# Kernel optimization log

Measured on AMD Instinct MI355X. Metric: run time of the kernel, lower is better.

The kernel has to match this reference:

```python
import jax, jax.numpy as jnp
import numpy as np

D_CUT = 5.0   # cosine-cutoff distance
SIZE = 128    # rbf size == hidden_channels (nn_dist size = in_channels)
L = 2         # num_layers
EPS = 0.0     # GIN eps (non-trainable, initial 0)


def _rbf(d):
    # d: (E,) distances -> (E, SIZE) expnorm RBF with cosine cutoff
    d = d[:, None]
    start = float(np.exp(-D_CUT))
    means = jnp.linspace(start, 1.0, SIZE)
    beta = (2.0 / SIZE * (1.0 - start)) ** (-2)
    dc = jnp.minimum(d, D_CUT)
    cutoff = 0.5 * (jnp.cos(dc * jnp.pi / D_CUT) + 1.0)
    return cutoff * jnp.exp(-beta * (jnp.exp(-d) - means) ** 2)


def setup_inputs() -> dict:
    key = jax.random.key(0)
    ks = jax.random.split(key, 40)
    it = iter(range(40))
    def k():
        return ks[next(it)]
    N, H, ED, AS = 100000, 128, 4, 4
    def w(shape, s):
        return jax.random.normal(k(), shape, jnp.float32) * s
    inp = {}
    inp['x_lig'] = jax.random.normal(k(), (N, H), jnp.float32)
    inp['x_pock'] = jax.random.normal(k(), (N, H), jnp.float32)
    for name, E in (('bond', 200000), ('lp', 400000), ('pl', 400000)):
        inp['ei_' + name] = jax.random.randint(k(), (2, E), 0, N, jnp.int32)
        inp['ew_' + name] = jax.random.uniform(k(), (E,), jnp.float32) * D_CUT
        inp['ea_' + name] = jax.random.normal(k(), (E, AS), jnp.float32)
    inp['W0'] = w((3, AS, ED), 0.5)                 # initial per-edge-type lins (no bias)
    inp['Wd'] = w((L, 3, H, 2 * H), H ** -0.5)      # RBFDistanceScaleShift lin
    inp['bd'] = jnp.zeros((L, 3, 2 * H), jnp.float32)
    inp['We'] = w((L, 3, ED, H), 0.5)               # EGINConv.lin (edge_dim -> hidden)
    inp['be'] = jnp.zeros((L, 3, H), jnp.float32)
    inp['W1'] = w((L, 3, H, H), H ** -0.5)          # nn_node MLP layer 1
    inp['b1'] = jnp.zeros((L, 3, H), jnp.float32)
    inp['W2'] = w((L, 3, H, H), H ** -0.5)          # nn_node MLP layer 2
    inp['b2'] = jnp.zeros((L, 3, H), jnp.float32)
    return inp


def reference(x_lig, x_pock, ei_bond, ew_bond, ea_bond, ei_lp, ew_lp, ea_lp,
              ei_pl, ew_pl, ea_pl, W0, Wd, bd, We, be, W1, b1, W2, b2):
    # HeteroEGIN.forward: initial per-edge-type linear on raw edge attrs (bias-free)
    ea0 = ea_bond @ W0[0]
    ea1 = ea_lp @ W0[1]
    ea2 = ea_pl @ W0[2]

    def conv(x_src, x_dst, ei, ew, ea, t, l):
        # EGINConv per edge type t, layer l
        ss = _rbf(ew) @ Wd[l, t] + bd[l, t]            # (E, 2H) scale/shift from distance
        scale, shift = jnp.split(ss, 2, axis=1)
        xj = x_src[ei[0]] + (ea @ We[l, t] + be[l, t])  # gather + edge-attr lin
        msg = jax.nn.relu(xj * scale + shift)           # gated message
        agg = jax.ops.segment_sum(msg, ei[1], num_segments=x_dst.shape[0])
        o = agg + (1.0 + EPS) * x_dst
        return jax.nn.relu(o @ W1[l, t] + b1[l, t]) @ W2[l, t] + b2[l, t]

    for l in range(L):
        # to_hetero: sum conv outputs across edge types per destination node type
        new_lig = (conv(x_lig, x_lig, ei_bond, ew_bond, ea0, 0, l)
                   + conv(x_pock, x_lig, ei_pl, ew_pl, ea2, 2, l))
        new_pock = conv(x_lig, x_pock, ei_lp, ew_lp, ea1, 1, l)
        if l < L - 1:  # BasicGNN: act between layers, none after last (jk=None)
            new_lig = jax.nn.relu(new_lig)
            new_pock = jax.nn.relu(new_pock)
        x_lig, x_pock = new_lig, new_pock
    return jnp.concatenate([x_lig, x_pock], axis=0)
```

## Files before the change

### kernel.cpp

```cpp
#include <hip/hip_runtime.h>
#include <hip/hip_bf16.h>
#include <hip/hip_fp16.h>
#include <cmath>

typedef __attribute__((ext_vector_type(8))) short short8_t;
typedef __attribute__((ext_vector_type(4))) float f32x4;

static __device__ __forceinline__ short f2bs(float f) {
    union { __hip_bfloat16 h; short s; } u;
    u.h = __float2bfloat16(f);
    return u.s;
}
static __device__ __forceinline__ float bs2f(unsigned int us) {
    union { float f; unsigned int i; } u;
    u.i = us << 16;
    return u.f;
}
static __device__ __forceinline__ unsigned int pack2bf(float a, float b) {
    return (unsigned int)(unsigned short)f2bs(a) |
           ((unsigned int)(unsigned short)f2bs(b) << 16);
}
static __device__ __forceinline__ void lds_barrier() {
    asm volatile("s_waitcnt lgkmcnt(0)\n\ts_barrier" ::: "memory");
}

__global__ void pack_kernel(const float* __restrict__ Wd,
                            const float* __restrict__ W1,
                            const float* __restrict__ W2,
                            const float* __restrict__ W0,
                            const float* __restrict__ We,
                            short* __restrict__ pWd,
                            short* __restrict__ pW1,
                            short* __restrict__ pW2,
                            float* __restrict__ Mb)
{
    const int tid = blockIdx.x * blockDim.x + threadIdx.x;
    const int stride = gridDim.x * blockDim.x;
    for (int i = tid; i < 6 * 32768; i += stride) {
        int c = i >> 15, rem = i & 32767;
        int f = rem >> 9, l = (rem >> 3) & 63, j = rem & 7;
        int kk = f >> 4, nt = f & 15;
        int k = kk * 32 + (l >> 4) * 8 + j;
        int n = nt * 16 + (l & 15);
        pWd[i] = f2bs(Wd[(size_t)c * 32768 + k * 256 + n]);
    }
    for (int i = tid; i < 6 * 16384; i += stride) {
        int c = i >> 14, rem = i & 16383;
        int f = rem >> 9, l = (rem >> 3) & 63, j = rem & 7;
        int kk = f >> 3, nt = f & 7;
        int k = kk * 32 + (l >> 4) * 8 + j;
        int n = nt * 16 + (l & 15);
        pW1[i] = f2bs(W1[(size_t)c * 16384 + k * 128 + n]);
        pW2[i] = f2bs(W2[(size_t)c * 16384 + k * 128 + n]);
    }
    for (int i = tid; i < 6 * 512; i += stride) {
        int c = i >> 9, rem = i & 511;
        int a = rem >> 7, h = rem & 127;
        int t = c % 3;
        float m = 0.f;
        #pragma unroll
        for (int j = 0; j < 4; ++j)
            m = fmaf(W0[t * 16 + a * 4 + j], We[(size_t)c * 512 + j * 128 + h], m);
        Mb[i] = m;
    }
}

__global__ void tobf16_kernel(const float* __restrict__ a, const float* __restrict__ b,
                              unsigned short* __restrict__ oa, unsigned short* __restrict__ ob,
                              int n4)
{
    int i = blockIdx.x * blockDim.x + threadIdx.x;
    const int stride = gridDim.x * blockDim.x;
    for (; i < n4; i += stride) {
        float4 va = ((const float4*)a)[i];
        uint2 pa; pa.x = pack2bf(va.x, va.y); pa.y = pack2bf(va.z, va.w);
        ((uint2*)oa)[i] = pa;
        float4 vb = ((const float4*)b)[i];
        uint2 pb; pb.x = pack2bf(vb.x, vb.y); pb.y = pack2bf(vb.z, vb.w);
        ((uint2*)ob)[i] = pb;
    }
}

__global__ __launch_bounds__(512, 2)
void edge_mfma_kernel(
    const unsigned short* __restrict__ xsb,
    const int* __restrict__ ei,
    const float* __restrict__ ew, const float* __restrict__ ea,
    const short* __restrict__ pWd, const float* __restrict__ bd,
    const float* __restrict__ Mb, const float* __restrict__ be,
    __half2* __restrict__ agg, int E, int ntiles,
    float rs, float rstep, float rbeta)
{
    __shared__ short sRbf[64 * 128];
    __shared__ __half sSS[64 * 256];

    const int t = threadIdx.x;
    const int lane = t & 63;
    const int w = t >> 6;
    const int l15 = lane & 15;
    const int l4 = lane >> 4;

    short8_t bfrag[4][2];
    #pragma unroll
    for (int kk = 0; kk < 4; ++kk)
        #pragma unroll
        for (int i = 0; i < 2; ++i)
            bfrag[kk][i] = *(const short8_t*)&pWd[((kk * 16 + 2 * w + i) * 64 + lane) * 8];
    float bdv[2];
    #pragma unroll
    for (int i = 0; i < 2; ++i) bdv[i] = bd[(2 * w + i) * 16 + l15];
    const float be0 = be[2 * lane], be1 = be[2 * lane + 1];
    float ma0[4], ma1[4];
    #pragma unroll
    for (int a = 0; a < 4; ++a) {
        ma0[a] = Mb[a * 128 + 2 * lane];
        ma1[a] = Mb[a * 128 + 2 * lane + 1];
    }

    const int stride = gridDim.x;
    int tile = blockIdx.x;
    if (tile >= ntiles) return;

    float dd_c; int dst_c; float4 ea_c;
    unsigned int gx[8];
    {
        const int e0 = tile << 6;
        int eL = e0 + lane;
        int eLc = eL < E ? eL : E - 1;
        dd_c = ew[eLc];
        int es = e0 + w * 8 + (lane & 7);
        int esv = es < E ? es : E - 1;
        dst_c = (es < E) ? ei[E + esv] : -1;
        int src_c = ei[esv];
        ea_c = *(const float4*)&ea[(size_t)esv * 4];
        #pragma unroll
        for (int r = 0; r < 8; ++r) {
            int srn = __shfl(src_c, r);
            gx[r] = *(const unsigned int*)&xsb[(size_t)srn * 128 + lane * 2];
        }
    }

    for (; tile < ntiles; tile += stride) {
        const float edv = __expf(-dd_c);
        const float dcc = fminf(dd_c, 5.0f);
        const float cutv = 0.5f * (__cosf(dcc * 0.62831853071795864769f) + 1.0f);
        {
            char* base = (char*)sRbf + lane * 256;
            #pragma unroll
            for (int c = 0; c < 2; ++c) {
                short8_t v;
                #pragma unroll
                for (int j = 0; j < 8; ++j) {
                    float mean = rs + (float)(w * 16 + c * 8 + j) * rstep;
                    float diff = edv - mean;
                    v[j] = f2bs(cutv * __expf(-rbeta * diff * diff));
                }
                *(short8_t*)(base + ((w * 32 + c * 16) ^ ((lane & 7) << 4))) = v;
            }
        }
        unsigned int xjr[8];
        #pragma unroll
        for (int r = 0; r < 8; ++r) {
            float ea0 = __shfl(ea_c.x, r), ea1 = __shfl(ea_c.y, r);
            float ea2 = __shfl(ea_c.z, r), ea3 = __shfl(ea_c.w, r);
            unsigned int g = gx[r];
            float x0 = bs2f(g & 0xffffu), x1 = bs2f(g >> 16);
            float o0 = x0 + be0 + ea0 * ma0[0] + ea1 * ma0[1] + ea2 * ma0[2] + ea3 * ma0[3];
            float o1 = x1 + be1 + ea0 * ma1[0] + ea1 * ma1[1] + ea2 * ma1[2] + ea3 * ma1[3];
            xjr[r] = pack2bf(o0, o1);
        }

        lds_barrier();

        const int ntile = tile + stride;
        const bool has_next = ntile < ntiles;
        float dd_n = 0.f; int dst_n = -1; int src_n = 0;
        float4 ea_n = {0.f, 0.f, 0.f, 0.f};
        if (has_next) {
            const int e0n = ntile << 6;
            int eL = e0n + lane;
            int eLc = eL < E ? eL : E - 1;
            dd_n = ew[eLc];
            int es = e0n + w * 8 + (lane & 7);
            int esv = es < E ? es : E - 1;
            dst_n = (es < E) ? ei[E + esv] : -1;
            src_n = ei[esv];
            ea_n = *(const float4*)&ea[(size_t)esv * 4];
        }
        __builtin_amdgcn_sched_barrier(0);

        f32x4 acc[4][2];
        #pragma unroll
        for (int m = 0; m < 4; ++m) {
            acc[m][0] = (f32x4){0.f, 0.f, 0.f, 0.f};
            acc[m][1] = (f32x4){0.f, 0.f, 0.f, 0.f};
        }
        #pragma unroll
        for (int kk = 0; kk < 4; ++kk) {
            short8_t af[4];
            #pragma unroll
            for (int m = 0; m < 4; ++m) {
                int row = m * 16 + l15;
                int byte = row * 256 + ((kk * 64 + l4 * 16) ^ ((row & 7) << 4));
                af[m] = *(const short8_t*)((const char*)sRbf + byte);
            }
            #pragma unroll
            for (int m = 0; m < 4; ++m)
                #pragma unroll
                for (int i = 0; i < 2; ++i)
                    acc[m][i] = __builtin_amdgcn_mfma_f32_16x16x32_bf16(
                        af[m], bfrag[kk][i], acc[m][i], 0, 0, 0);
        }

        #pragma unroll
        for (int m = 0; m < 4; ++m)
            #pragma unroll
            for (int i = 0; i < 2; ++i) {
                int col = (2 * w + i) * 16 + l15;
                #pragma unroll
                for (int r = 0; r < 4; ++r) {
                    int row = m * 16 + l4 * 4 + r;
                    int byte = row * 512 + ((col * 2) ^ ((row & 7) << 4));
                    *(__half*)((char*)sSS + byte) = __float2half(acc[m][i][r] + bdv[i]);
                }
            }

        if (has_next) {
            #pragma unroll
            for (int r = 0; r < 8; ++r) {
                int srn = __shfl(src_n, r);
                gx[r] = *(const unsigned int*)&xsb[(size_t)srn * 128 + lane * 2];
            }
        }
        const int dst_f = dst_c;
        dd_c = dd_n; dst_c = dst_n; ea_c = ea_n;

        lds_barrier();

        #pragma unroll
        for (int r = 0; r < 8; ++r) {
            int e = 8 * w + r;
            int dst = __shfl(dst_f, r);
            unsigned int sc = *(const unsigned int*)
                ((const char*)sSS + e * 512 + ((lane * 4) ^ ((e & 7) << 4)));
            unsigned int sh = *(const unsigned int*)
                ((const char*)sSS + e * 512 + ((256 + lane * 4) ^ ((e & 7) << 4)));
            float2 scf = __half22float2(*(const __half2*)&sc);
            float2 shf = __half22float2(*(const __half2*)&sh);
            unsigned int g = xjr[r];
            float x0 = bs2f(g & 0xffffu), x1 = bs2f(g >> 16);
            float m0 = fmaxf(fmaf(x0, scf.x, shf.x), 0.0f);
            float m1 = fmaxf(fmaf(x1, scf.y, shf.y), 0.0f);
            __half2 hv = __floats2half2_rn(m0, m1);
            unsigned int hbits = *(unsigned int*)&hv;
            if (dst >= 0 && hbits != 0u)
                unsafeAtomicAdd(agg + (size_t)dst * 64 + lane, hv);
        }
    }
}

__global__ __launch_bounds__(256)
void node_mfma_kernel(
    const __half2* __restrict__ agg,
    const float* __restrict__ xdf, const unsigned short* __restrict__ xdb,
    const short* __restrict__ pW1, const float* __restrict__ b1,
    const short* __restrict__ pW2, const float* __restrict__ b2,
    float* __restrict__ outf, unsigned short* __restrict__ outb,
    int N, int ntiles, int accumulate, int relu_out)
{
    __shared__ short sA[64 * 128];
    __shared__ short sH[64 * 128];

    const int t = threadIdx.x;
    const int lane = t & 63;
    const int w = t >> 6;
    const int l15 = lane & 15;
    const int l4 = lane >> 4;

    short8_t w1f[4][2], w2f[4][2];
    #pragma unroll
    for (int kk = 0; kk < 4; ++kk)
        #pragma unroll
        for (int p = 0; p < 2; ++p) {
            int nt = 2 * w + p;
            w1f[kk][p] = *(const short8_t*)&pW1[((kk * 8 + nt) * 64 + lane) * 8];
            w2f[kk][p] = *(const short8_t*)&pW2[((kk * 8 + nt) * 64 + lane) * 8];
        }
    float b1v[2], b2v[2];
    #pragma unroll
    for (int p = 0; p < 2; ++p) {
        int col = (2 * w + p) * 16 + l15;
        b1v[p] = b1[col];
        b2v[p] = b2[col];
    }

    for (int tile = blockIdx.x; tile < ntiles; tile += gridDim.x) {
        const int n0 = tile << 6;
        #pragma unroll
        for (int i = 0; i < 4; ++i) {
            int idx = i * 256 + t;
            int row = idx >> 4, c8 = idx & 15;
            int gr = n0 + row; if (gr >= N) gr = N - 1;
            union { float4 f; __half2 h[4]; } ar;
            ar.f = ((const float4*)agg)[(size_t)gr * 16 + c8];
            float xv[8];
            if (xdf) {
                float4 x0 = ((const float4*)xdf)[(size_t)gr * 32 + c8 * 2];
                float4 x1 = ((const float4*)xdf)[(size_t)gr * 32 + c8 * 2 + 1];
                xv[0] = x0.x; xv[1] = x0.y; xv[2] = x0.z; xv[3] = x0.w;
                xv[4] = x1.x; xv[5] = x1.y; xv[6] = x1.z; xv[7] = x1.w;
            } else {
                uint4 xr = ((const uint4*)xdb)[(size_t)gr * 16 + c8];
                xv[0] = bs2f(xr.x & 0xffffu); xv[1] = bs2f(xr.x >> 16);
                xv[2] = bs2f(xr.y & 0xffffu); xv[3] = bs2f(xr.y >> 16);
                xv[4] = bs2f(xr.z & 0xffffu); xv[5] = bs2f(xr.z >> 16);
                xv[6] = bs2f(xr.w & 0xffffu); xv[7] = bs2f(xr.w >> 16);
            }
            short8_t v;
            #pragma unroll
            for (int j = 0; j < 4; ++j) {
                float2 a2 = __half22float2(ar.h[j]);
                v[2 * j]     = f2bs(a2.x + xv[2 * j]);
                v[2 * j + 1] = f2bs(a2.y + xv[2 * j + 1]);
            }
            int byte = row * 256 + ((c8 * 16) ^ ((row & 7) << 4));
            *(short8_t*)((char*)sA + byte) = v;
        }
        lds_barrier();

        f32x4 acc[4][2];
        #pragma unroll
        for (int m = 0; m < 4; ++m) {
            acc[m][0] = (f32x4){0.f, 0.f, 0.f, 0.f};
            acc[m][1] = (f32x4){0.f, 0.f, 0.f, 0.f};
        }
        #pragma unroll
        for (int kk = 0; kk < 4; ++kk) {
            short8_t af[4];
            #pragma unroll
            for (int m = 0; m < 4; ++m) {
                int row = m * 16 + l15;
                int byte = row * 256 + ((kk * 64 + l4 * 16) ^ ((row & 7) << 4));
                af[m] = *(const short8_t*)((const char*)sA + byte);
            }
            #pragma unroll
            for (int m = 0; m < 4; ++m)
                #pragma unroll
                for (int p = 0; p < 2; ++p)
                    acc[m][p] = __builtin_amdgcn_mfma_f32_16x16x32_bf16(
                        af[m], w1f[kk][p], acc[m][p], 0, 0, 0);
        }
        #pragma unroll
        for (int m = 0; m < 4; ++m)
            #pragma unroll
            for (int p = 0; p < 2; ++p) {
                int col = (2 * w + p) * 16 + l15;
                #pragma unroll
                for (int r = 0; r < 4; ++r) {
                    int row = m * 16 + l4 * 4 + r;
                    short hs = f2bs(fmaxf(acc[m][p][r] + b1v[p], 0.f));
                    int byte = row * 256 + ((col * 2) ^ ((row & 7) << 4));
                    *(short*)((char*)sH + byte) = hs;
                }
            }
        lds_barrier();

        f32x4 acc2[4][2];
        #pragma unroll
        for (int m = 0; m < 4; ++m) {
            acc2[m][0] = (f32x4){0.f, 0.f, 0.f, 0.f};
            acc2[m][1] = (f32x4){0.f, 0.f, 0.f, 0.f};
        }
        #pragma unroll
        for (int kk = 0; kk < 4; ++kk) {
            short8_t af[4];
            #pragma unroll
            for (int m = 0; m < 4; ++m) {
                int row = m * 16 + l15;
                int byte = row * 256 + ((kk * 64 + l4 * 16) ^ ((row & 7) << 4));
                af[m] = *(const short8_t*)((const char*)sH + byte);
            }
            #pragma unroll
            for (int m = 0; m < 4; ++m)
                #pragma unroll
                for (int p = 0; p < 2; ++p)
                    acc2[m][p] = __builtin_amdgcn_mfma_f32_16x16x32_bf16(
                        af[m], w2f[kk][p], acc2[m][p], 0, 0, 0);
        }
        #pragma unroll
        for (int m = 0; m < 4; ++m)
            #pragma unroll
            for (int p = 0; p < 2; ++p) {
                int col = (2 * w + p) * 16 + l15;
                #pragma unroll
                for (int r = 0; r < 4; ++r) {
                    int row = n0 + m * 16 + l4 * 4 + r;
                    if (row < N) {
                        float v = acc2[m][p][r] + b2v[p];
                        if (outf) {
                            float* op = &outf[(size_t)row * 128 + col];
                            if (accumulate) v += *op;
                            if (relu_out) v = fmaxf(v, 0.f);
                            *op = v;
                        } else {
                            unsigned short* op = &outb[(size_t)row * 128 + col];
                            if (accumulate) v += bs2f((unsigned int)*op);
                            if (relu_out) v = fmaxf(v, 0.f);
                            *op = (unsigned short)f2bs(v);
                        }
                    }
                }
            }
    }
}

extern "C" void kernel_launch(void* const* d_in, const int* in_sizes, int n_in,
                              void* d_out, int out_size, void* d_ws, size_t ws_size,
                              hipStream_t stream)
{
    const float* x_lig   = (const float*)d_in[0];
    const float* x_pock  = (const float*)d_in[1];
    const int*   ei_bond = (const int*)d_in[2];
    const float* ew_bond = (const float*)d_in[3];
    const float* ea_bond = (const float*)d_in[4];
    const int*   ei_lp   = (const int*)d_in[5];
    const float* ew_lp   = (const float*)d_in[6];
    const float* ea_lp   = (const float*)d_in[7];
    const int*   ei_pl   = (const int*)d_in[8];
    const float* ew_pl   = (const float*)d_in[9];
    const float* ea_pl   = (const float*)d_in[10];
    const float* W0 = (const float*)d_in[11];
    const float* Wd = (const float*)d_in[12];
    const float* bd = (const float*)d_in[13];
    const float* We = (const float*)d_in[14];
    const float* be = (const float*)d_in[15];
    const float* W1 = (const float*)d_in[16];
    const float* b1 = (const float*)d_in[17];
    const float* W2 = (const float*)d_in[18];
    const float* b2 = (const float*)d_in[19];

    const int H = 128;
    const int N = in_sizes[0] / H;
    const int E_bond = in_sizes[3];
    const int E_lp   = in_sizes[6];
    const int E_pl   = in_sizes[9];

    unsigned short* A  = (unsigned short*)d_ws;
    unsigned short* Bb = A  + (size_t)N * H;
    unsigned short* C  = Bb + (size_t)N * H;
    __half* agg = (__half*)(C + (size_t)N * H);
    short* pWd  = (short*)(agg + (size_t)N * H);
    short* pW1s = pWd + 6 * 32768;
    short* pW2s = pW1s + 6 * 16384;
    float* Mb   = (float*)(pW2s + 6 * 16384);

    float* outL = (float*)d_out;
    float* outP = outL + (size_t)N * H;

    const int capE = 2 * 256;
    const int capN = 4 * 256;

    tobf16_kernel<<<512, 256, 0, stream>>>(x_lig, x_pock, A, Bb, N * H / 4);
    pack_kernel<<<256, 256, 0, stream>>>(Wd, W1, W2, W0, We, pWd, pW1s, pW2s, Mb);

    const double start_d = exp(-5.0);
    const float rs    = (float)start_d;
    const float rstep = (float)((1.0 - start_d) / 127.0);
    const float rbeta = (float)std::pow(2.0 / 128.0 * (1.0 - start_d), -2.0);

    auto conv = [&](const unsigned short* src,
                    const float* xdf, const unsigned short* xdb,
                    const int* ei_, const float* ew_, const float* ea_, int E,
                    int l, int tt, float* outf, unsigned short* outb,
                    int accum, int relu) {
        hipMemsetAsync(agg, 0, (size_t)N * H * sizeof(__half), stream);
        const int lt = l * 3 + tt;
        const int ntE = (E + 63) / 64;
        const int gE = ntE < capE ? ntE : capE;
        edge_mfma_kernel<<<gE, 512, 0, stream>>>(
            src, ei_, ew_, ea_,
            pWd + (size_t)lt * 32768, bd + (size_t)lt * 256,
            Mb + (size_t)lt * 512, be + (size_t)lt * 128,
            (__half2*)agg, E, ntE, rs, rstep, rbeta);
        const int ntN = (N + 63) / 64;
        const int gN = ntN < capN ? ntN : capN;
        node_mfma_kernel<<<gN, 256, 0, stream>>>(
            (const __half2*)agg, xdf, xdb,
            pW1s + (size_t)lt * 16384, b1 + (size_t)lt * 128,
            pW2s + (size_t)lt * 16384, b2 + (size_t)lt * 128,
            outf, outb, N, ntN, accum, relu);
    };

    conv(A,  x_pock, nullptr, ei_lp,   ew_lp,   ea_lp,   E_lp,   0, 1, nullptr, C, 0, 1);
    conv(A,  x_lig,  nullptr, ei_bond, ew_bond, ea_bond, E_bond, 0, 0, nullptr, A, 0, 0);
    conv(Bb, x_lig,  nullptr, ei_pl,   ew_pl,   ea_pl,   E_pl,   0, 2, nullptr, A, 1, 1);
    conv(A, nullptr, A, ei_bond, ew_bond, ea_bond, E_bond, 1, 0, outL, nullptr, 0, 0);
    conv(C, nullptr, A, ei_pl,   ew_pl,   ea_pl,   E_pl,   1, 2, outL, nullptr, 1, 0);
    conv(A, nullptr, C, ei_lp,   ew_lp,   ea_lp,   E_lp,   1, 1, outP, nullptr, 0, 0);
}
```

Baseline: 851.8 us.

## Counting-sort edges by destination and combine same-destination messages before atomics

```diff
diff --git a/kernel.cpp b/kernel.cpp
--- a/kernel.cpp
+++ b/kernel.cpp
@@ -81,11 +81,62 @@
     }
 }
 
+__global__ void hist_kernel(const int* __restrict__ ei, int* __restrict__ cnt, int E)
+{
+    for (int e = blockIdx.x * blockDim.x + threadIdx.x; e < E;
+         e += gridDim.x * blockDim.x)
+        atomicAdd(&cnt[ei[E + e]], 1);
+}
+
+__global__ void scan1k_kernel(int* __restrict__ data, int* __restrict__ bsum, int n)
+{
+    __shared__ int buf[1024];
+    const int gid = blockIdx.x * 1024 + threadIdx.x;
+    int v = (gid < n) ? data[gid] : 0;
+    buf[threadIdx.x] = v;
+    __syncthreads();
+    for (int off = 1; off < 1024; off <<= 1) {
+        int t = (threadIdx.x >= off) ? buf[threadIdx.x - off] : 0;
+        __syncthreads();
+        buf[threadIdx.x] += t;
+        __syncthreads();
+    }
+    if (gid < n) data[gid] = buf[threadIdx.x] - v;
+    if (bsum && threadIdx.x == 1023) bsum[blockIdx.x] = buf[1023];
+}
+
+__global__ void scan_add_kernel(int* __restrict__ data, const int* __restrict__ bsum,
+                                int* __restrict__ cursor, int n)
+{
+    const int gid = blockIdx.x * 1024 + threadIdx.x;
+    if (gid < n) {
+        int v = data[gid] + bsum[blockIdx.x];
+        data[gid] = v;
+        cursor[gid] = v;
+    }
+}
+
+__global__ void scatter_kernel(const int* __restrict__ ei, const float* __restrict__ ew,
+                               const float4* __restrict__ ea, int* __restrict__ cursor,
+                               float* __restrict__ ewp, float4* __restrict__ eap,
+                               int* __restrict__ srcp, int* __restrict__ dstp, int E)
+{
+    for (int e = blockIdx.x * blockDim.x + threadIdx.x; e < E;
+         e += gridDim.x * blockDim.x) {
+        int d = ei[E + e];
+        int p = atomicAdd(&cursor[d], 1);
+        ewp[p]  = ew[e];
+        eap[p]  = ea[e];
+        srcp[p] = ei[e];
+        dstp[p] = d;
+    }
+}
+
 __global__ __launch_bounds__(512, 2)
 void edge_mfma_kernel(
     const unsigned short* __restrict__ xsb,
-    const int* __restrict__ ei,
-    const float* __restrict__ ew, const float* __restrict__ ea,
+    const int* __restrict__ srcp, const int* __restrict__ dstp,
+    const float* __restrict__ ewp, const float4* __restrict__ eap,
     const short* __restrict__ pWd, const float* __restrict__ bd,
     const float* __restrict__ Mb, const float* __restrict__ be,
     __half2* __restrict__ agg, int E, int ntiles,
@@ -127,12 +178,12 @@
         const int e0 = tile << 6;
         int eL = e0 + lane;
         int eLc = eL < E ? eL : E - 1;
-        dd_c = ew[eLc];
+        dd_c = ewp[eLc];
         int es = e0 + w * 8 + (lane & 7);
         int esv = es < E ? es : E - 1;
-        dst_c = (es < E) ? ei[E + esv] : -1;
-        int src_c = ei[esv];
-        ea_c = *(const float4*)&ea[(size_t)esv * 4];
+        dst_c = (es < E) ? dstp[esv] : -1;
+        int src_c = srcp[esv];
+        ea_c = eap[esv];
         #pragma unroll
         for (int r = 0; r < 8; ++r) {
             int srn = __shfl(src_c, r);
@@ -180,12 +231,12 @@
             const int e0n = ntile << 6;
             int eL = e0n + lane;
             int eLc = eL < E ? eL : E - 1;
-            dd_n = ew[eLc];
+            dd_n = ewp[eLc];
             int es = e0n + w * 8 + (lane & 7);
             int esv = es < E ? es : E - 1;
-            dst_n = (es < E) ? ei[E + esv] : -1;
-            src_n = ei[esv];
-            ea_n = *(const float4*)&ea[(size_t)esv * 4];
+            dst_n = (es < E) ? dstp[esv] : -1;
+            src_n = srcp[esv];
+            ea_n = eap[esv];
         }
         __builtin_amdgcn_sched_barrier(0);
 
@@ -237,24 +288,42 @@
 
         lds_barrier();
 
-        #pragma unroll
-        for (int r = 0; r < 8; ++r) {
-            int e = 8 * w + r;
-            int dst = __shfl(dst_f, r);
-            unsigned int sc = *(const unsigned int*)
-                ((const char*)sSS + e * 512 + ((lane * 4) ^ ((e & 7) << 4)));
-            unsigned int sh = *(const unsigned int*)
-                ((const char*)sSS + e * 512 + ((256 + lane * 4) ^ ((e & 7) << 4)));
-            float2 scf = __half22float2(*(const __half2*)&sc);
-            float2 shf = __half22float2(*(const __half2*)&sh);
-            unsigned int g = xjr[r];
-            float x0 = bs2f(g & 0xffffu), x1 = bs2f(g >> 16);
-            float m0 = fmaxf(fmaf(x0, scf.x, shf.x), 0.0f);
-            float m1 = fmaxf(fmaf(x1, scf.y, shf.y), 0.0f);
-            __half2 hv = __floats2half2_rn(m0, m1);
-            unsigned int hbits = *(unsigned int*)&hv;
-            if (dst >= 0 && hbits != 0u)
-                unsafeAtomicAdd(agg + (size_t)dst * 64 + lane, hv);
+        {
+            float a0 = 0.f, a1 = 0.f;
+            int rdst = __shfl(dst_f, 0);
+            #pragma unroll
+            for (int r = 0; r < 8; ++r) {
+                int e = 8 * w + r;
+                unsigned int sc = *(const unsigned int*)
+                    ((const char*)sSS + e * 512 + ((lane * 4) ^ ((e & 7) << 4)));
+                unsigned int sh = *(const unsigned int*)
+                    ((const char*)sSS + e * 512 + ((256 + lane * 4) ^ ((e & 7) << 4)));
+                float2 scf = __half22float2(*(const __half2*)&sc);
+                float2 shf = __half22float2(*(const __half2*)&sh);
+                unsigned int g = xjr[r];
+                float x0 = bs2f(g & 0xffffu), x1 = bs2f(g >> 16);
+                float m0 = fmaxf(fmaf(x0, scf.x, shf.x), 0.0f);
+                float m1 = fmaxf(fmaf(x1, scf.y, shf.y), 0.0f);
+                int d = __shfl(dst_f, r);
+                if (d != rdst) {
+                    if (rdst >= 0) {
+                        __half2 hv = __floats2half2_rn(a0, a1);
+                        unsigned int hb;
+                        __builtin_memcpy(&hb, &hv, 4);
+                        if (hb)
+                            unsafeAtomicAdd(agg + (size_t)rdst * 64 + lane, hv);
+                    }
+                    a0 = 0.f; a1 = 0.f; rdst = d;
+                }
+                a0 += m0; a1 += m1;
+            }
+            if (rdst >= 0) {
+                __half2 hv = __floats2half2_rn(a0, a1);
+                unsigned int hb;
+                __builtin_memcpy(&hb, &hv, 4);
+                if (hb)
+                    unsafeAtomicAdd(agg + (size_t)rdst * 64 + lane, hv);
+            }
         }
     }
 }
@@ -445,14 +514,35 @@
     const int E_lp   = in_sizes[6];
     const int E_pl   = in_sizes[9];
 
-    unsigned short* A  = (unsigned short*)d_ws;
-    unsigned short* Bb = A  + (size_t)N * H;
-    unsigned short* C  = Bb + (size_t)N * H;
-    __half* agg = (__half*)(C + (size_t)N * H);
-    short* pWd  = (short*)(agg + (size_t)N * H);
-    short* pW1s = pWd + 6 * 32768;
-    short* pW2s = pW1s + 6 * 16384;
-    float* Mb   = (float*)(pW2s + 6 * 16384);
+    char* wp = (char*)d_ws;
+    auto alloc = [&](size_t bytes) -> char* {
+        char* r = wp;
+        wp += (bytes + 255) & ~(size_t)255;
+        return r;
+    };
+    unsigned short* A   = (unsigned short*)alloc((size_t)N * H * 2);
+    unsigned short* Bb  = (unsigned short*)alloc((size_t)N * H * 2);
+    unsigned short* C   = (unsigned short*)alloc((size_t)N * H * 2);
+    __half*  agg  = (__half*)alloc((size_t)N * H * 2);
+    float4*  eapB = (float4*)alloc((size_t)E_bond * 16);
+    float4*  eapL = (float4*)alloc((size_t)E_lp * 16);
+    float4*  eapP = (float4*)alloc((size_t)E_pl * 16);
+    float*   ewpB = (float*)alloc((size_t)E_bond * 4);
+    float*   ewpL = (float*)alloc((size_t)E_lp * 4);
+    float*   ewpP = (float*)alloc((size_t)E_pl * 4);
+    int*     srcB = (int*)alloc((size_t)E_bond * 4);
+    int*     srcL = (int*)alloc((size_t)E_lp * 4);
+    int*     srcP = (int*)alloc((size_t)E_pl * 4);
+    int*     dstB = (int*)alloc((size_t)E_bond * 4);
+    int*     dstL = (int*)alloc((size_t)E_lp * 4);
+    int*     dstP = (int*)alloc((size_t)E_pl * 4);
+    short*   pWd  = (short*)alloc(6 * 32768 * 2);
+    short*   pW1s = (short*)alloc(6 * 16384 * 2);
+    short*   pW2s = (short*)alloc(6 * 16384 * 2);
+    float*   Mb   = (float*)alloc(6 * 512 * 4);
+    int*     cnt    = (int*)alloc((size_t)N * 4);
+    int*     cursor = (int*)alloc((size_t)N * 4);
+    int*     bsum   = (int*)alloc(1024 * 4);
 
     float* outL = (float*)d_out;
     float* outP = outL + (size_t)N * H;
@@ -462,6 +552,21 @@
 
     tobf16_kernel<<<512, 256, 0, stream>>>(x_lig, x_pock, A, Bb, N * H / 4);
     pack_kernel<<<256, 256, 0, stream>>>(Wd, W1, W2, W0, We, pWd, pW1s, pW2s, Mb);
+
+    const int nb = (N + 1023) / 1024;
+    auto sortset = [&](const int* ei_, const float* ew_, const float* ea_, int E,
+                       float* ewp, float4* eap, int* sr716, int* dstp) {
+        hipMemsetAsync(cnt, 0, (size_t)N * sizeof(int), stream);
+        hist_kernel<<<512, 256, 0, stream>>>(ei_, cnt, E);
+        scan1k_kernel<<<nb, 1024, 0, stream>>>(cnt, bsum, N);
+        scan1k_kernel<<<1, 1024, 0, stream>>>(bsum, nullptr, nb);
+        scan_add_kernel<<<nb, 1024, 0, stream>>>(cnt, bsum, cursor, N);
+        scatter_kernel<<<512, 256, 0, stream>>>(ei_, ew_, (const float4*)ea_,
+                                                cursor, ewp, eap, sr716, dstp, E);
+    };
+    sortset(ei_bond, ew_bond, ea_bond, E_bond, ewpB, eapB, srcB, dstB);
+    sortset(ei_lp,   ew_lp,   ea_lp,   E_lp,   ewpL, eapL, srcL, dstL);
+    sortset(ei_pl,   ew_pl,   ea_pl,   E_pl,   ewpP, eapP, srcP, dstP);
 
     const double start_d = exp(-5.0);
     const float rs    = (float)start_d;
@@ -470,7 +575,8 @@
 
     auto conv = [&](const unsigned short* src,
                     const float* xdf, const unsigned short* xdb,
-                    const int* ei_, const float* ew_, const float* ea_, int E,
+                    const int* srcp, const int* dstp, const float* ewp,
+                    const float4* eap, int E,
                     int l, int tt, float* outf, unsigned short* outb,
                     int accum, int relu) {
         hipMemsetAsync(agg, 0, (size_t)N * H * sizeof(__half), stream);
@@ -478,7 +584,7 @@
         const int ntE = (E + 63) / 64;
         const int gE = ntE < capE ? ntE : capE;
         edge_mfma_kernel<<<gE, 512, 0, stream>>>(
-            src, ei_, ew_, ea_,
+            src, srcp, dstp, ewp, eap,
             pWd + (size_t)lt * 32768, bd + (size_t)lt * 256,
             Mb + (size_t)lt * 512, be + (size_t)lt * 128,
             (__half2*)agg, E, ntE, rs, rstep, rbeta);
@@ -491,10 +597,10 @@
             outf, outb, N, ntN, accum, relu);
     };
 
-    conv(A,  x_pock, nullptr, ei_lp,   ew_lp,   ea_lp,   E_lp,   0, 1, nullptr, C, 0, 1);
-    conv(A,  x_lig,  nullptr, ei_bond, ew_bond, ea_bond, E_bond, 0, 0, nullptr, A, 0, 0);
-    conv(Bb, x_lig,  nullptr, ei_pl,   ew_pl,   ea_pl,   E_pl,   0, 2, nullptr, A, 1, 1);
-    conv(A, nullptr, A, ei_bond, ew_bond, ea_bond, E_bond, 1, 0, outL, nullptr, 0, 0);
-    conv(C, nullptr, A, ei_pl,   ew_pl,   ea_pl,   E_pl,   1, 2, outL, nullptr, 1, 0);
-    conv(A, nullptr, C, ei_lp,   ew_lp,   ea_lp,   E_lp,   1, 1, outP, nullptr, 0, 0);
-}
+    conv(A,  x_pock, nullptr, srcL, dstL, ewpL, eapL, E_lp,   0, 1, nullptr, C, 0, 1);
+    conv(A,  x_lig,  nullptr, srcB, dstB, ewpB, eapB, E_bond, 0, 0, nullptr, A, 0, 0);
+    conv(Bb, x_lig,  nullptr, srcP, dstP, ewpP, eapP, E_pl,   0, 2, nullptr, A, 1, 1);
+    conv(A, nullptr, A, srcB, dstB, ewpB, eapB, E_bond, 1, 0, outL, nullptr, 0, 0);
+    conv(C, nullptr, A, srcP, dstP, ewpP, eapP, E_pl,   1, 2, outL, nullptr, 1, 0);
+    conv(A, nullptr, C, srcL, dstL, ewpL, eapL, E_lp,   1, 1, outP, nullptr, 0, 0);
+}
```

Measured after the change: 936.2 us. +9.9%, slower.
